# Optimization experiments

Measured on AMD Instinct MI355X. Metric: run time of the kernel, lower is better.

## Reference

```python
import jax, jax.numpy as jnp
import numpy as np

N = 150    # MAXSIZE tokens per sentence
D = 1024   # emb_dim == d_model (hard-asserted in the torch code)
R = 92     # 46 dep labels + 46 'r-' reversed labels
E = 450    # total (token, dep-type) edges, ~3 deps/token
SCALE = float(np.sqrt(2.0 / 7.0))  # torch init: rand(...) * sqrt(2/7)


def setup_inputs() -> dict:
    key = jax.random.key(0)
    k = jax.random.split(key, 5)
    x = jax.random.normal(k[0], (N, D), dtype=jnp.float32)
    W_pos = jax.random.uniform(k[1], (N, D, D), dtype=jnp.float32) * SCALE
    b_pos = jnp.ones((N, D), dtype=jnp.float32)   # torch bias is ones((1, emb_dim)) per position
    W_dep = jax.random.uniform(k[2], (R, D, D), dtype=jnp.float32) * SCALE
    b_dep = jnp.ones((R, D), dtype=jnp.float32)
    edge_token = jax.random.randint(k[3], (E,), 0, N, dtype=jnp.int32)
    edge_type = jax.random.randint(k[4], (E,), 0, R, dtype=jnp.int32)
    return {"x": x, "W_pos": W_pos, "b_pos": b_pos, "W_dep": W_dep,
            "b_dep": b_dep, "edge_token": edge_token, "edge_type": edge_type}


def reference(x, W_pos, b_pos, W_dep, b_dep, edge_token, edge_type):
    # counts[n, r] = number of deps of type r attached to token n
    counts = jnp.zeros((x.shape[0], W_dep.shape[0]), dtype=x.dtype)
    counts = counts.at[edge_token, edge_type].add(jnp.ones_like(edge_token, dtype=x.dtype))
    # per-position self term: x_n @ W_pos[n] + b_pos[n]
    self_out = jnp.einsum('nd,nde->ne', x, W_pos) + b_pos
    # dep term: sum over attached deps of x_n @ W_dep[r] + b_dep[r]
    dep_all = jnp.einsum('nd,rde->nre', x, W_dep)        # [N, R, D]
    dep_out = jnp.einsum('nre,nr->ne', dep_all, counts) + counts @ b_dep
    return jax.nn.relu(self_out + dep_out)
```

## Files before the change

kernel.cpp:

```cpp
#include <hip/hip_runtime.h>
#include <cstdint>
#include <cstddef>

#define D   1024
#define DC  128
#define TG  16

__device__ __forceinline__ void fma4(float4& a, float s, const float4& w) {
    a.x = fmaf(s, w.x, a.x);
    a.y = fmaf(s, w.y, a.y);
    a.z = fmaf(s, w.z, a.z);
    a.w = fmaf(s, w.w, a.w);
}

__global__ void build_lists(const int* __restrict__ etok,
                            const int* __restrict__ etyp,
                            float* __restrict__ counts,
                            int* __restrict__ tcnt,
                            int* __restrict__ tlist,
                            int E, int R) {
    int i = blockIdx.x * blockDim.x + threadIdx.x;
    if (i < E) {
        int n = etok[i];
        int r = etyp[i];
        atomicAdd(&counts[(size_t)n * R + r], 1.0f);
        int idx = atomicAdd(&tcnt[r], 1);
        tlist[(size_t)r * E + idx] = n;
    }
}

__global__ void __launch_bounds__(256)
self_kernel(const float* __restrict__ x,
            const float* __restrict__ Wpos,
            float* __restrict__ acc) {
    const int n  = blockIdx.x;
    const int d0 = blockIdx.y * DC;
    const int tid = threadIdx.x;

    __shared__ float xs[DC];
    if (tid < DC) xs[tid] = x[(size_t)n * D + d0 + tid];
    __syncthreads();

    const int e = tid * 4;
    const float* W = Wpos + ((size_t)n * D + d0) * D + e;

    float4 a = {0.f, 0.f, 0.f, 0.f};
    #pragma unroll 4
    for (int dd = 0; dd < DC; dd += 4) {
        const float4 xv = *(const float4*)&xs[dd];
        const float* Wd = W + (size_t)dd * D;
        float4 w0 = *(const float4*)(Wd);
        float4 w1 = *(const float4*)(Wd + D);
        float4 w2 = *(const float4*)(Wd + 2 * D);
        float4 w3 = *(const float4*)(Wd + 3 * D);
        fma4(a, xv.x, w0);
        fma4(a, xv.y, w1);
        fma4(a, xv.z, w2);
        fma4(a, xv.w, w3);
    }

    float* o = acc + (size_t)n * D + e;
    atomicAdd(o + 0, a.x);
    atomicAdd(o + 1, a.y);
    atomicAdd(o + 2, a.z);
    atomicAdd(o + 3, a.w);
}

__global__ void __launch_bounds__(256)
dep_kernel(const float* __restrict__ x,
           const float* __restrict__ Wdep,
           const int* __restrict__ tcnt,
           const int* __restrict__ tlist,
           float* __restrict__ acc,
           int E) {
    const int r  = blockIdx.x;
    const int d0 = blockIdx.y * DC;
    const int cnt = tcnt[r];
    if (cnt == 0) return;

    const int tid = threadIdx.x;
    const int e = tid * 4;

    __shared__ float xs[DC][TG];
    __shared__ int   toks[TG];

    const float* W = Wdep + ((size_t)r * D + d0) * D + e;

    for (int base = 0; base < cnt; base += TG) {
        const int m = min(TG, cnt - base);

        __syncthreads();
        if (tid < TG) {
            toks[tid] = (tid < m) ? tlist[(size_t)r * E + base + tid] : -1;
        }
        for (int k = tid; k < DC * TG; k += 256) {
            const int dd = k >> 4;
            const int i  = k & (TG - 1);
            float v = 0.f;
            if (i < m) {
                const int t = tlist[(size_t)r * E + base + i];
                v = x[(size_t)t * D + d0 + dd];
            }
            xs[dd][i] = v;
        }
        __syncthreads();

        float4 a[TG];
        #pragma unroll
        for (int i = 0; i < TG; ++i) a[i] = make_float4(0.f, 0.f, 0.f, 0.f);

        for (int dd = 0; dd < DC; ++dd) {
            const float4 w = *(const float4*)(W + (size_t)dd * D);
            #pragma unroll
            for (int i4 = 0; i4 < TG / 4; ++i4) {
                const float4 xv = *(const float4*)&xs[dd][i4 * 4];
                fma4(a[i4 * 4 + 0], xv.x, w);
                fma4(a[i4 * 4 + 1], xv.y, w);
                fma4(a[i4 * 4 + 2], xv.z, w);
                fma4(a[i4 * 4 + 3], xv.w, w);
            }
        }

        #pragma unroll
        for (int i = 0; i < TG; ++i) {
            if (i < m) {
                const int t = toks[i];
                float* o = acc + (size_t)t * D + e;
                atomicAdd(o + 0, a[i].x);
                atomicAdd(o + 1, a[i].y);
                atomicAdd(o + 2, a[i].z);
                atomicAdd(o + 3, a[i].w);
            }
        }
    }
}

__global__ void __launch_bounds__(256)
final_kernel(const float* __restrict__ acc,
             const float* __restrict__ bpos,
             const float* __restrict__ bdep,
             const float* __restrict__ counts,
             float* __restrict__ out,
             int R) {
    const int n = blockIdx.x;
    const int e = threadIdx.x * 4;

    float4 a  = *(const float4*)(acc  + (size_t)n * D + e);
    const float4 bp = *(const float4*)(bpos + (size_t)n * D + e);
    a.x += bp.x; a.y += bp.y; a.z += bp.z; a.w += bp.w;

    const float* cn = counts + (size_t)n * R;
    for (int r = 0; r < R; ++r) {
        const float cr = cn[r];
        if (cr != 0.0f) {
            const float4 bd = *(const float4*)(bdep + (size_t)r * D + e);
            fma4(a, cr, bd);
        }
    }

    float4 o;
    o.x = fmaxf(a.x, 0.f);
    o.y = fmaxf(a.y, 0.f);
    o.z = fmaxf(a.z, 0.f);
    o.w = fmaxf(a.w, 0.f);
    *(float4*)(out + (size_t)n * D + e) = o;
}

extern "C" void kernel_launch(void* const* d_in, const int* in_sizes, int n_in,
                              void* d_out, int out_size, void* d_ws, size_t ws_size,
                              hipStream_t stream) {
    const float* x    = (const float*)d_in[0];
    const float* Wpos = (const float*)d_in[1];
    const float* bpos = (const float*)d_in[2];
    const float* Wdep = (const float*)d_in[3];
    const float* bdep = (const float*)d_in[4];
    const int*   etok = (const int*)d_in[5];
    const int*   etyp = (const int*)d_in[6];
    float* out = (float*)d_out;

    const int N = in_sizes[0] / D;
    const int R = in_sizes[4] / D;
    const int E = in_sizes[5];

    float* acc    = (float*)d_ws;
    float* counts = acc + (size_t)N * D;
    int*   tcnt   = (int*)(counts + (size_t)N * R);
    int*   tlist  = tcnt + R;

    const size_t zero_bytes = ((size_t)N * D + (size_t)N * R + (size_t)R) * sizeof(float);
    hipMemsetAsync(d_ws, 0, zero_bytes, stream);

    build_lists<<<(E + 255) / 256, 256, 0, stream>>>(etok, etyp, counts, tcnt, tlist, E, R);
    self_kernel<<<dim3(N, D / DC), 256, 0, stream>>>(x, Wpos, acc);
    dep_kernel<<<dim3(R, D / DC), 256, 0, stream>>>(x, Wdep, tcnt, tlist, acc, E);
    final_kernel<<<N, 256, 0, stream>>>(acc, bpos, bdep, counts, out, R);
}
```

Before: 1.092 ms.

## Replace float atomics with per-chunk partial buffers reduced in final kernel

Instead of atomically accumulating self and dep contributions into a shared accumulator, each D-chunk writes its partial result to a dedicated slot (per position for self, per edge for dep). The final kernel sums the chunk partials and walks a per-token edge list to add dep partials and biases. This removes atomic traffic and the large memset, at the cost of extra partial-buffer writes and reads (about 8x(N+E)xD floats) and a serial per-token edge loop in the final kernel. It also makes the accumulation order deterministic.

```diff
diff --git a/kernel.cpp b/kernel.cpp
--- a/kernel.cpp
+++ b/kernel.cpp
@@ -2,9 +2,10 @@
 #include <cstdint>
 #include <cstddef>
 
-#define D   1024
-#define DC  128
-#define TG  16
+#define D    1024
+#define DC   128
+#define NCH  (D / DC)
+#define TG   16
 
 __device__ __forceinline__ void fma4(float4& a, float s, const float4& w) {
     a.x = fmaf(s, w.x, a.x);
@@ -15,26 +16,30 @@
 
 __global__ void build_lists(const int* __restrict__ etok,
                             const int* __restrict__ etyp,
-                            float* __restrict__ counts,
                             int* __restrict__ tcnt,
                             int* __restrict__ tlist,
-                            int E, int R) {
+                            int* __restrict__ ncnt,
+                            int* __restrict__ nlist,
+                            int E) {
     int i = blockIdx.x * blockDim.x + threadIdx.x;
     if (i < E) {
         int n = etok[i];
         int r = etyp[i];
-        atomicAdd(&counts[(size_t)n * R + r], 1.0f);
-        int idx = atomicAdd(&tcnt[r], 1);
-        tlist[(size_t)r * E + idx] = n;
+        int k  = atomicAdd(&tcnt[r], 1);
+        tlist[(size_t)r * E + k] = i;
+        int k2 = atomicAdd(&ncnt[n], 1);
+        nlist[(size_t)n * E + k2] = i;
     }
 }
 
 __global__ void __launch_bounds__(256)
 self_kernel(const float* __restrict__ x,
             const float* __restrict__ Wpos,
-            float* __restrict__ acc) {
+            float* __restrict__ Pself,
+            int N) {
     const int n  = blockIdx.x;
-    const int d0 = blockIdx.y * DC;
+    const int c  = blockIdx.y;
+    const int d0 = c * DC;
     const int tid = threadIdx.x;
 
     __shared__ float xs[DC];
@@ -59,22 +64,20 @@
         fma4(a, xv.w, w3);
     }
 
-    float* o = acc + (size_t)n * D + e;
-    atomicAdd(o + 0, a.x);
-    atomicAdd(o + 1, a.y);
-    atomicAdd(o + 2, a.z);
-    atomicAdd(o + 3, a.w);
+    *(float4*)(Pself + ((size_t)c * N + n) * D + e) = a;
 }
 
 __global__ void __launch_bounds__(256)
 dep_kernel(const float* __restrict__ x,
            const float* __restrict__ Wdep,
+           const int* __restrict__ etok,
            const int* __restrict__ tcnt,
            const int* __restrict__ tlist,
-           float* __restrict__ acc,
+           float* __restrict__ Pdep,
            int E) {
     const int r  = blockIdx.x;
-    const int d0 = blockIdx.y * DC;
+    const int c  = blockIdx.y;
+    const int d0 = c * DC;
     const int cnt = tcnt[r];
     if (cnt == 0) return;
 
@@ -82,7 +85,7 @@
     const int e = tid * 4;
 
     __shared__ float xs[DC][TG];
-    __shared__ int   toks[TG];
+    __shared__ int   eids[TG];
 
     const float* W = Wdep + ((size_t)r * D + d0) * D + e;
 
@@ -91,14 +94,15 @@
 
         __syncthreads();
         if (tid < TG) {
-            toks[tid] = (tid < m) ? tlist[(size_t)r * E + base + tid] : -1;
+            eids[tid] = (tid < m) ? tlist[(size_t)r * E + base + tid] : -1;
         }
         for (int k = tid; k < DC * TG; k += 256) {
             const int dd = k >> 4;
             const int i  = k & (TG - 1);
             float v = 0.f;
             if (i < m) {
-                const int t = tlist[(size_t)r * E + base + i];
+                const int eid = tlist[(size_t)r * E + base + i];
+                const int t   = etok[eid];
                 v = x[(size_t)t * D + d0 + dd];
             }
             xs[dd][i] = v;
@@ -124,37 +128,43 @@
         #pragma unroll
         for (int i = 0; i < TG; ++i) {
             if (i < m) {
-                const int t = toks[i];
-                float* o = acc + (size_t)t * D + e;
-                atomicAdd(o + 0, a[i].x);
-                atomicAdd(o + 1, a[i].y);
-                atomicAdd(o + 2, a[i].z);
-                atomicAdd(o + 3, a[i].w);
+                *(float4*)(Pdep + ((size_t)c * E + eids[i]) * D + e) = a[i];
             }
         }
     }
 }
 
 __global__ void __launch_bounds__(256)
-final_kernel(const float* __restrict__ acc,
+final_kernel(const float* __restrict__ Pself,
+             const float* __restrict__ Pdep,
              const float* __restrict__ bpos,
              const float* __restrict__ bdep,
-             const float* __restrict__ counts,
+             const int* __restrict__ etyp,
+             const int* __restrict__ ncnt,
+             const int* __restrict__ nlist,
              float* __restrict__ out,
-             int R) {
+             int N, int E) {
     const int n = blockIdx.x;
     const int e = threadIdx.x * 4;
 
-    float4 a  = *(const float4*)(acc  + (size_t)n * D + e);
-    const float4 bp = *(const float4*)(bpos + (size_t)n * D + e);
-    a.x += bp.x; a.y += bp.y; a.z += bp.z; a.w += bp.w;
-
-    const float* cn = counts + (size_t)n * R;
-    for (int r = 0; r < R; ++r) {
-        const float cr = cn[r];
-        if (cr != 0.0f) {
-            const float4 bd = *(const float4*)(bdep + (size_t)r * D + e);
-            fma4(a, cr, bd);
+    float4 a = *(const float4*)(bpos + (size_t)n * D + e);
+
+    #pragma unroll
+    for (int c = 0; c < NCH; ++c) {
+        const float4 p = *(const float4*)(Pself + ((size_t)c * N + n) * D + e);
+        a.x += p.x; a.y += p.y; a.z += p.z; a.w += p.w;
+    }
+
+    const int deg = ncnt[n];
+    for (int k = 0; k < deg; ++k) {
+        const int i = nlist[(size_t)n * E + k];
+        const int r = etyp[i];
+        const float4 bd = *(const float4*)(bdep + (size_t)r * D + e);
+        a.x += bd.x; a.y += bd.y; a.z += bd.z; a.w += bd.w;
+        #pragma unroll
+        for (int c = 0; c < NCH; ++c) {
+            const float4 p = *(const float4*)(Pdep + ((size_t)c * E + i) * D + e);
+            a.x += p.x; a.y += p.y; a.z += p.z; a.w += p.w;
         }
     }
 
@@ -182,16 +192,17 @@
     const int R = in_sizes[4] / D;
     const int E = in_sizes[5];
 
-    float* acc    = (float*)d_ws;
-    float* counts = acc + (size_t)N * D;
-    int*   tcnt   = (int*)(counts + (size_t)N * R);
-    int*   tlist  = tcnt + R;
-
-    const size_t zero_bytes = ((size_t)N * D + (size_t)N * R + (size_t)R) * sizeof(float);
-    hipMemsetAsync(d_ws, 0, zero_bytes, stream);
-
-    build_lists<<<(E + 255) / 256, 256, 0, stream>>>(etok, etyp, counts, tcnt, tlist, E, R);
-    self_kernel<<<dim3(N, D / DC), 256, 0, stream>>>(x, Wpos, acc);
-    dep_kernel<<<dim3(R, D / DC), 256, 0, stream>>>(x, Wdep, tcnt, tlist, acc, E);
-    final_kernel<<<N, 256, 0, stream>>>(acc, bpos, bdep, counts, out, R);
-}
+    float* Pself = (float*)d_ws;
+    float* Pdep  = Pself + (size_t)NCH * N * D;
+    int*   tcnt  = (int*)(Pdep + (size_t)NCH * E * D);
+    int*   ncnt  = tcnt + R;
+    int*   tlist = ncnt + N;
+    int*   nlist = tlist + (size_t)R * E;
+
+    hipMemsetAsync(tcnt, 0, (size_t)(R + N) * sizeof(int), stream);
+
+    build_lists<<<(E + 255) / 256, 256, 0, stream>>>(etok, etyp, tcnt, tlist, ncnt, nlist, E);
+    self_kernel<<<dim3(N, NCH), 256, 0, stream>>>(x, Wpos, Pself, N);
+    dep_kernel<<<dim3(R, NCH), 256, 0, stream>>>(x, Wdep, etok, tcnt, tlist, Pdep, E);
+    final_kernel<<<N, 256, 0, stream>>>(Pself, Pdep, bpos, bdep, etyp, ncnt, nlist, out, N, E);
+}
```

After: 1.027 ms. -5.9%, faster.
